# Optimization experiments

Measured on AMD Instinct MI355X. Metric: run time of the kernel, lower is better.

Reference implementation:

```python
import jax, jax.numpy as jnp
import numpy as np


def setup_inputs() -> dict:
    key = jax.random.key(0)
    ks = jax.random.split(key, 5)
    B, C_in, C_out, H, W, k = 16, 64, 64, 256, 256, 16
    scale = 1.0 / (C_in * C_out)
    return {
        "u": jax.random.normal(ks[0], (B, C_in, H, W), dtype=jnp.float32),
        "W_pos_re": scale * jax.random.normal(ks[1], (C_in, C_out, k, k), dtype=jnp.float32),
        "W_pos_im": scale * jax.random.normal(ks[2], (C_in, C_out, k, k), dtype=jnp.float32),
        "W_neg_re": scale * jax.random.normal(ks[3], (C_in, C_out, k, k), dtype=jnp.float32),
        "W_neg_im": scale * jax.random.normal(ks[4], (C_in, C_out, k, k), dtype=jnp.float32),
    }


def reference(u, W_pos_re, W_pos_im, W_neg_re, W_neg_im):
    B, C_in, H, W = u.shape
    C_out = W_pos_re.shape[1]
    k = W_pos_re.shape[2]
    W_half = W // 2 + 1
    k_h = min(k, H // 2)
    k_w = min(k, W_half)

    R_pos = (W_pos_re + 1j * W_pos_im)[:, :, :k_h, :k_w]  # (C_in, C_out, k_h, k_w)
    R_neg = (W_neg_re + 1j * W_neg_im)[:, :, :k_h, :k_w]

    u_hat = jnp.fft.rfft2(u, norm="ortho")  # (B, C_in, H, W_half) complex

    # spectral multiply on retained modes only
    top = jnp.einsum("bchw,cohw->bohw", u_hat[:, :, :k_h, :k_w], R_pos)
    bot = jnp.einsum("bchw,cohw->bohw", u_hat[:, :, H - k_h:, :k_w], R_neg)

    v_hat = jnp.zeros((B, C_out, H, W_half), dtype=u_hat.dtype)
    v_hat = v_hat.at[:, :, :k_h, :k_w].set(top)
    v_hat = v_hat.at[:, :, H - k_h:, :k_w].set(bot)

    return jnp.fft.irfft2(v_hat, s=(H, W), norm="ortho")  # (B, C_out, H, W) real
```

## Files before the change

kernel.cpp:

```cpp
#include <hip/hip_runtime.h>


#define OFF_CT 0
#define OFF_ST 256
#define OFF_RP 512
#define RP_SZ  (512*4096*2)
#define OFF_U  (OFF_RP + RP_SZ)
#define U_SZ   (1024*512*2)
#define OFF_V  (OFF_U + U_SZ)

#define UTP   260
#define TWOPI_256 0.024543692606170259f

typedef const __attribute__((address_space(1))) void g_void;
typedef __attribute__((address_space(3))) void l_void;

__device__ __forceinline__ void load_lds16(const float* g, float* l) {
    __builtin_amdgcn_global_load_lds((g_void*)g, (l_void*)l, 16, 0, 0);
}

template<int CTRL>
__device__ __forceinline__ float dppf(float x) {
    return __int_as_float(__builtin_amdgcn_update_dpp(
        0, __float_as_int(x), CTRL, 0xF, 0xF, true));
}

__global__ __launch_bounds__(256) void k_fwd1(const float* __restrict__ u,
                                              const float* __restrict__ wpr,
                                              const float* __restrict__ wpi,
                                              const float* __restrict__ wnr,
                                              const float* __restrict__ wni,
                                              float* __restrict__ ws,
                                              float* __restrict__ P) {
    __shared__ __align__(16) float ut[32][UTP];
    int t = threadIdx.x;

    if (blockIdx.x >= 8192) {
        int mw = blockIdx.x - 8192;
        int m = mw >> 4, wmc = mw & 15;
        const float* wr; const float* wi; int i;
        if (m < 16) { wr = wpr; wi = wpi; i = m; }
        else        { wr = wnr; wi = wni; i = m - 16; }
        if (mw == 0) {
            double a = 2.0 * 3.14159265358979323846 * (double)t / 256.0;
            ws[OFF_CT + t] = (float)cos(a);
            ws[OFF_ST + t] = (float)sin(a);
        }
        float norm = (wmc == 0 ? 1.f : 2.f) * (1.f / 65536.f);
        int off = i * 16 + wmc;
        float2* rp = (float2*)(ws + OFF_RP) + (size_t)mw * 4096;
        #pragma unroll
        for (int k = 0; k < 16; ++k) {
            int co = t + 256 * k;
            rp[co] = make_float2(wr[(size_t)co * 256 + off] * norm,
                                 wi[(size_t)co * 256 + off] * norm);
        }
        return;
    }

    int bc = blockIdx.x >> 3, ch = blockIdx.x & 7;
    const float* ub = u + (size_t)bc * 65536 + ch * 8192;
    int lane = t & 63, w = t >> 6;
    #pragma unroll
    for (int k = 0; k < 8; ++k)
        load_lds16(ub + (w * 8 + k) * 256 + lane * 4, &ut[w * 8 + k][0]);

    int s = lane & 3, h = (lane >> 2) & 1, r8 = lane >> 3;
    int rowc = w * 8 + r8;

    float sv, cv;
    __sincosf(TWOPI_256 * 1.f, &sv, &cv);
    float rb1r = cv, rb1i = -sv;
    __sincosf(TWOPI_256 * (float)(8 * h), &sv, &cv);
    float r8hr = cv, r8hi = -sv;
    int j0 = 16 * s;
    __sincosf(TWOPI_256 * (float)((8 * h * j0) & 255), &sv, &cv);
    float tw0r = cv, tw0i = -sv;
    __sincosf(TWOPI_256 * (float)j0, &sv, &cv);
    float bjr = cv, bji = -sv;

    float a0r=0,a0i=0,a1r=0,a1i=0,a2r=0,a2i=0,a3r=0,a3i=0;
    float a4r=0,a4i=0,a5r=0,a5i=0,a6r=0,a6i=0,a7r=0,a7i=0;

    asm volatile("s_waitcnt vmcnt(0)" ::: "memory");

    const float* q0p = &ut[rowc][j0];
    #define CMUL_(tr_, ti_) { float nr_ = tr_*bjr - ti_*bji,                \
          ni_ = tr_*bji + ti_*bjr; tr_ = nr_; ti_ = ni_; }
    #define STEP_(u0,u1,u2,u3) {                                            \
        float Av_=(u0)+(u2), Bv_=(u1)+(u3), Cv_=(u0)-(u2), Dv_=(u1)-(u3);   \
        float gp_ = Av_ + Bv_, gm_ = Av_ - Bv_;                             \
        float twr = tw0r, twi = tw0i;                                       \
        a0r = fmaf(gp_, twr, a0r); a0i = fmaf(gp_, twi, a0i);               \
        CMUL_(twr, twi)                                                     \
        a1r = fmaf(Cv_, twr, fmaf( Dv_, twi, a1r));                         \
        a1i = fmaf(Cv_, twi, fmaf(-Dv_, twr, a1i));                         \
        CMUL_(twr, twi)                                                     \
        a2r = fmaf(gm_, twr, a2r); a2i = fmaf(gm_, twi, a2i);               \
        CMUL_(twr, twi)                                                     \
        a3r = fmaf(Cv_, twr, fmaf(-Dv_, twi, a3r));                         \
        a3i = fmaf(Cv_, twi, fmaf( Dv_, twr, a3i));                         \
        CMUL_(twr, twi)                                                     \
        a4r = fmaf(gp_, twr, a4r); a4i = fmaf(gp_, twi, a4i);               \
        CMUL_(twr, twi)                                                     \
        a5r = fmaf(Cv_, twr, fmaf( Dv_, twi, a5r));                         \
        a5i = fmaf(Cv_, twi, fmaf(-Dv_, twr, a5i));                         \
        CMUL_(twr, twi)                                                     \
        a6r = fmaf(gm_, twr, a6r); a6i = fmaf(gm_, twi, a6i);               \
        CMUL_(twr, twi)                                                     \
        a7r = fmaf(Cv_, twr, fmaf(-Dv_, twi, a7r));                         \
        a7i = fmaf(Cv_, twi, fmaf( Dv_, twr, a7i));                         \
        { float nr = tw0r*r8hr - tw0i*r8hi, ni = tw0r*r8hi + tw0i*r8hr;     \
          tw0r = nr; tw0i = ni; }                                           \
        { float nr = bjr*rb1r - bji*rb1i, ni = bjr*rb1i + bji*rb1r;         \
          bjr = nr; bji = ni; } }

    #pragma unroll
    for (int g = 0; g < 4; ++g) {
        float4 x0 = *(const float4*)(q0p + 4 * g);
        float4 x1 = *(const float4*)(q0p + 64  + 4 * g);
        float4 x2 = *(const float4*)(q0p + 128 + 4 * g);
        float4 x3 = *(const float4*)(q0p + 192 + 4 * g);
        STEP_(x0.x, x1.x, x2.x, x3.x)
        STEP_(x0.y, x1.y, x2.y, x3.y)
        STEP_(x0.z, x1.z, x2.z, x3.z)
        STEP_(x0.w, x1.w, x2.w, x3.w)
    }
    #undef STEP_
    #undef CMUL_

    #define RED_(v) { v += dppf<0xB1>(v); v += dppf<0x4E>(v); }
    RED_(a0r) RED_(a0i) RED_(a1r) RED_(a1i)
    RED_(a2r) RED_(a2i) RED_(a3r) RED_(a3i)
    RED_(a4r) RED_(a4i) RED_(a5r) RED_(a5i)
    RED_(a6r) RED_(a6i) RED_(a7r) RED_(a7i)
    #undef RED_

    if ((lane & 3) == 0) {
        int y = ch * 32 + rowc;
        float4* Pp = (float4*)P + (((size_t)bc * 256 + y) * 8 + 4 * h);
        Pp[0] = make_float4(a0r, a0i, a1r, a1i);
        Pp[1] = make_float4(a2r, a2i, a3r, a3i);
        Pp[2] = make_float4(a4r, a4i, a5r, a5i);
        Pp[3] = make_float4(a6r, a6i, a7r, a7i);
    }
}

__global__ __launch_bounds__(256) void k_fwd2(const float* __restrict__ P,
                                              float* __restrict__ ws) {
    __shared__ float Pl[256][36];
    int t = threadIdx.x, bc = blockIdx.x;
    const float4* Pg = (const float4*)(P + (size_t)bc * 8192);
    #pragma unroll
    for (int k = 0; k < 8; ++k) {
        int f4 = t + 256 * k;
        int y = f4 >> 3, q = f4 & 7;
        *(float4*)&Pl[y][q * 4] = Pg[f4];
    }
    __syncthreads();

    int wm = t & 15;
    int v  = t >> 4;
    int m1 = ((v & 3) << 2) | (v >> 2);
    float sv, cv;
    __sincosf(TWOPI_256 * (float)m1, &sv, &cv);
    float r1r = cv, r1i = -sv;
    __sincosf(TWOPI_256 * (float)(m1 - 16), &sv, &cv);
    float r2r = cv, r2i = -sv;
    float t1r = 1.f, t1i = 0.f, t2r = 1.f, t2i = 0.f;
    float U1r = 0.f, U1i = 0.f, U2r = 0.f, U2i = 0.f;
    int md = m1 & 3;
    #pragma unroll 4
    for (int yy = 0; yy < 64; ++yy) {
        float2 P0 = *(float2*)&Pl[yy][2 * wm];
        float2 P1 = *(float2*)&Pl[yy + 64][2 * wm];
        float2 P2 = *(float2*)&Pl[yy + 128][2 * wm];
        float2 P3 = *(float2*)&Pl[yy + 192][2 * wm];
        float ar = P0.x + P2.x, ai = P0.y + P2.y;
        float br = P1.x + P3.x, bi = P1.y + P3.y;
        float cr = P0.x - P2.x, ci = P0.y - P2.y;
        float dr = P1.x - P3.x, di = P1.y - P3.y;
        float gr, gi;
        if (md == 0)      { gr = ar + br; gi = ai + bi; }
        else if (md == 1) { gr = cr + di; gi = ci - dr; }
        else if (md == 2) { gr = ar - br; gi = ai - bi; }
        else              { gr = cr - di; gi = ci + dr; }
        U1r = fmaf(gr, t1r, fmaf(-gi, t1i, U1r));
        U1i = fmaf(gr, t1i, fmaf( gi, t1r, U1i));
        U2r = fmaf(gr, t2r, fmaf(-gi, t2i, U2r));
        U2i = fmaf(gr, t2i, fmaf( gi, t2r, U2i));
        float n1r = t1r * r1r - t1i * r1i, n1i = t1r * r1i + t1i * r1r;
        float n2r = t2r * r2r - t2i * r2i, n2i = t2r * r2i + t2i * r2r;
        t1r = n1r; t1i = n1i; t2r = n2r; t2i = n2i;
    }
    float2* U = (float2*)(ws + OFF_U) + (size_t)bc * 512;
    U[m1 * 16 + wm]          = make_float2(U1r, U1i);
    U[(m1 + 16) * 16 + wm]   = make_float2(U2r, U2i);
}

__global__ __launch_bounds__(256) void k_cgemm(float* __restrict__ ws) {
    __shared__ float2 Ul[1024];
    int mw = blockIdx.x, t = threadIdx.x;
    const float2* Ug = (const float2*)(ws + OFF_U);
    #pragma unroll
    for (int k = 0; k < 4; ++k) {
        int bcv = t + 256 * k;
        Ul[bcv] = Ug[(size_t)bcv * 512 + mw];
    }
    __syncthreads();
    int o = t & 63, bq = t >> 6;
    const float2* rp = (const float2*)(ws + OFF_RP) + (size_t)mw * 4096;
    float ar[4] = {0.f, 0.f, 0.f, 0.f}, ai[4] = {0.f, 0.f, 0.f, 0.f};
    #pragma unroll 4
    for (int c = 0; c < 64; ++c) {
        float2 R = rp[c * 64 + o];
        #pragma unroll
        for (int j = 0; j < 4; ++j) {
            float2 Uv = Ul[(bq * 4 + j) * 64 + c];
            ar[j] = fmaf(Uv.x, R.x, fmaf(-Uv.y, R.y, ar[j]));
            ai[j] = fmaf(Uv.x, R.y, fmaf( Uv.y, R.x, ai[j]));
        }
    }
    float2* Vg = (float2*)(ws + OFF_V) + (size_t)mw * 1024;
    #pragma unroll
    for (int j = 0; j < 4; ++j)
        Vg[(bq * 4 + j) * 64 + o] = make_float2(ar[j], ai[j]);
}

__global__ __launch_bounds__(256) void k_inv(const float* __restrict__ ws,
                                             float* __restrict__ out) {
    __shared__ float Vl[16][68];
    __shared__ float Tl[4][16][36];
    __shared__ float ct[256], st[256];
    int t = threadIdx.x;
    int bo = blockIdx.x >> 2, q = blockIdx.x & 3;
    ct[t] = ws[OFF_CT + t];
    st[t] = ws[OFF_ST + t];
    {
        const float2* Vg = (const float2*)(ws + OFF_V);
        float2 v0 = Vg[(size_t)t * 1024 + bo];
        float2 v1 = Vg[(size_t)(t + 256) * 1024 + bo];
        int m = t >> 4, wmv = t & 15;
        Vl[wmv][2 * m]        = v0.x;  Vl[wmv][2 * m + 1]        = v0.y;
        Vl[wmv][2 * (m + 16)] = v1.x;  Vl[wmv][2 * (m + 16) + 1] = v1.y;
    }
    __syncthreads();

    int wm4 = t & 15, yb = t >> 4;
    int y0 = q * 16 + yb;
    float vr[32], vi[32];
    #pragma unroll
    for (int m = 0; m < 32; ++m) { vr[m] = Vl[wm4][2 * m]; vi[m] = Vl[wm4][2 * m + 1]; }
    float cy = ct[y0], sy = st[y0];
    float T0r=0,T0i=0,T1r=0,T1i=0,T2r=0,T2i=0,T3r=0,T3i=0;
    float tr = 1.f, ti = 0.f;
    #pragma unroll
    for (int m = 0; m < 32; ++m) {
        if (m == 16) {
            int i16 = (4096 - 16 * y0) & 255;
            tr = ct[i16]; ti = st[i16];
        }
        float hr = vr[m] * tr - vi[m] * ti;
        float hi = vr[m] * ti + vi[m] * tr;
        const int md = m & 3;
        T0r += hr; T0i += hi;
        if (md == 0)      { T1r += hr; T1i += hi; T2r += hr; T2i += hi; T3r += hr; T3i += hi; }
        else if (md == 1) { T1r -= hi; T1i += hr; T2r -= hr; T2i -= hi; T3r += hi; T3i -= hr; }
        else if (md == 2) { T1r -= hr; T1i -= hi; T2r += hr; T2i += hi; T3r -= hr; T3i -= hi; }
        else              { T1r += hi; T1i -= hr; T2r -= hr; T2i -= hi; T3r -= hi; T3i += hr; }
        float nr = tr * cy - ti * sy, ni = tr * sy + ti * cy;
        tr = nr; ti = ni;
    }
    Tl[0][yb][wm4] = T0r; Tl[0][yb][16 + wm4] = T0i;
    Tl[1][yb][wm4] = T1r; Tl[1][yb][16 + wm4] = T1i;
    Tl[2][yb][wm4] = T2r; Tl[2][yb][16 + wm4] = T2i;
    Tl[3][yb][wm4] = T3r; Tl[3][yb][16 + wm4] = T3i;
    __syncthreads();

    int l = t & 63, wv = t >> 6;
    float c0[16], s0[16];
    #pragma unroll
    for (int wm = 0; wm < 16; ++wm) {
        int idx = (wm * l) & 255;
        c0[wm] = ct[idx]; s0[wm] = st[idx];
    }
    float* ob = out + (size_t)bo * 65536;
    for (int yi = 0; yi < 16; ++yi) {
        int y = wv * 64 + q * 16 + yi;
        float TR[16], TI[16];
        const float4* rowv = (const float4*)&Tl[wv][yi][0];
        #pragma unroll
        for (int qq = 0; qq < 4; ++qq) {
            float4 a = rowv[qq];
            TR[4*qq]=a.x; TR[4*qq+1]=a.y; TR[4*qq+2]=a.z; TR[4*qq+3]=a.w;
            float4 b = rowv[qq + 4];
            TI[4*qq]=b.x; TI[4*qq+1]=b.y; TI[4*qq+2]=b.z; TI[4*qq+3]=b.w;
        }
        float Pv = 0.f, Qv = 0.f, Rv = 0.f, Sv = 0.f;
        #pragma unroll
        for (int wm = 0; wm < 16; wm += 2) {
            Pv = fmaf(TR[wm],     c0[wm],     Pv);
            Rv = fmaf(TI[wm],     s0[wm],     Rv);
            Qv = fmaf(TR[wm + 1], c0[wm + 1], Qv);
            Sv = fmaf(TI[wm + 1], s0[wm + 1], Sv);
        }
        float Ac = Pv + Qv, Bs = Rv + Sv;
        float Dc = Pv - Qv, Es = Rv - Sv;
        float* row = ob + (size_t)y * 256;
        row[l]               = Ac - Bs;
        row[(256 - l) & 255] = Ac + Bs;
        row[128 + l]         = Dc - Es;
        row[128 - l]         = Dc + Es;
        float E0 = TR[0] + TR[4] + TR[8]  + TR[12];
        float E2 = TR[2] + TR[6] + TR[10] + TR[14];
        float O1 = TI[1] + TI[5] + TI[9]  + TI[13];
        float O3 = TI[3] + TI[7] + TI[11] + TI[15];
        float EC = E0 - E2, OC = O1 - O3;
        if (l == 0) {
            row[64]  = EC - OC;
            row[192] = EC + OC;
        }
    }
}

extern "C" void kernel_launch(void* const* d_in, const int* in_sizes, int n_in,
                              void* d_out, int out_size, void* d_ws, size_t ws_size,
                              hipStream_t stream) {
    const float* u   = (const float*)d_in[0];
    const float* wpr = (const float*)d_in[1];
    const float* wpi = (const float*)d_in[2];
    const float* wnr = (const float*)d_in[3];
    const float* wni = (const float*)d_in[4];
    float* out = (float*)d_out;
    float* ws  = (float*)d_ws;
    float* P   = (float*)d_out;

    hipLaunchKernelGGL(k_fwd1,  dim3(8704), dim3(256), 0, stream, u, wpr, wpi, wnr, wni, ws, P);
    hipLaunchKernelGGL(k_fwd2,  dim3(1024), dim3(256), 0, stream, P, ws);
    hipLaunchKernelGGL(k_cgemm, dim3(512),  dim3(256), 0, stream, ws);
    hipLaunchKernelGGL(k_inv,   dim3(4096), dim3(256), 0, stream, ws, out);
}
```

Before: 204.7 us.

## Fuse column DFT stage into forward row-DFT kernel with partial sums

Removes the separate k_fwd2 kernel. Each k_fwd1 block now does its 32-row slice of the column DFT directly from shared memory and writes per-chunk partial spectra. k_cgemm sums the 8 partial chunks while loading. This drops one kernel launch and the round trip of the full row-DFT intermediate through global memory. In exchange, the partial-sum buffer is 8x the size of the retained spectrum, cgemm does extra strided loads, and the fwd1 blocks get extra shared memory and a sync.

```diff
diff --git a/kernel.cpp b/kernel.cpp
--- a/kernel.cpp
+++ b/kernel.cpp
@@ -5,9 +5,7 @@
 #define OFF_ST 256
 #define OFF_RP 512
 #define RP_SZ  (512*4096*2)
-#define OFF_U  (OFF_RP + RP_SZ)
-#define U_SZ   (1024*512*2)
-#define OFF_V  (OFF_U + U_SZ)
+#define OFF_V  (OFF_RP + RP_SZ)
 
 #define UTP   260
 #define TWOPI_256 0.024543692606170259f
@@ -31,8 +29,9 @@
                                               const float* __restrict__ wnr,
                                               const float* __restrict__ wni,
                                               float* __restrict__ ws,
-                                              float* __restrict__ P) {
+                                              float* __restrict__ Upart) {
     __shared__ __align__(16) float ut[32][UTP];
+    __shared__ __align__(16) float Pl[32][36];
     int t = threadIdx.x;
 
     if (blockIdx.x >= 8192) {
@@ -82,6 +81,15 @@
     float a0r=0,a0i=0,a1r=0,a1i=0,a2r=0,a2i=0,a3r=0,a3i=0;
     float a4r=0,a4i=0,a5r=0,a5i=0,a6r=0,a6i=0,a7r=0,a7i=0;
 
+    int wm2 = t & 15, m1 = t >> 4;
+    __sincosf(TWOPI_256 * (float)m1, &sv, &cv);
+    float q1r = cv, q1i = -sv;
+    __sincosf(TWOPI_256 * (float)(m1 - 16), &sv, &cv);
+    float q2r = cv, q2i = -sv;
+    __sincosf(TWOPI_256 * (float)((m1 * 32 * ch) & 255), &sv, &cv);
+    float w1r = cv, w1i = -sv;
+    float w2r = w1r, w2i = w1i;
+
     asm volatile("s_waitcnt vmcnt(0)" ::: "memory");
 
     const float* q0p = &ut[rowc][j0];
@@ -137,75 +145,46 @@
     #undef RED_
 
     if ((lane & 3) == 0) {
-        int y = ch * 32 + rowc;
-        float4* Pp = (float4*)P + (((size_t)bc * 256 + y) * 8 + 4 * h);
+        float4* Pp = (float4*)&Pl[rowc][16 * h];
         Pp[0] = make_float4(a0r, a0i, a1r, a1i);
         Pp[1] = make_float4(a2r, a2i, a3r, a3i);
         Pp[2] = make_float4(a4r, a4i, a5r, a5i);
         Pp[3] = make_float4(a6r, a6i, a7r, a7i);
     }
-}
-
-__global__ __launch_bounds__(256) void k_fwd2(const float* __restrict__ P,
-                                              float* __restrict__ ws) {
-    __shared__ float Pl[256][36];
-    int t = threadIdx.x, bc = blockIdx.x;
-    const float4* Pg = (const float4*)(P + (size_t)bc * 8192);
-    #pragma unroll
-    for (int k = 0; k < 8; ++k) {
-        int f4 = t + 256 * k;
-        int y = f4 >> 3, q = f4 & 7;
-        *(float4*)&Pl[y][q * 4] = Pg[f4];
-    }
     __syncthreads();
 
-    int wm = t & 15;
-    int v  = t >> 4;
-    int m1 = ((v & 3) << 2) | (v >> 2);
-    float sv, cv;
-    __sincosf(TWOPI_256 * (float)m1, &sv, &cv);
-    float r1r = cv, r1i = -sv;
-    __sincosf(TWOPI_256 * (float)(m1 - 16), &sv, &cv);
-    float r2r = cv, r2i = -sv;
-    float t1r = 1.f, t1i = 0.f, t2r = 1.f, t2i = 0.f;
     float U1r = 0.f, U1i = 0.f, U2r = 0.f, U2i = 0.f;
-    int md = m1 & 3;
     #pragma unroll 4
-    for (int yy = 0; yy < 64; ++yy) {
-        float2 P0 = *(float2*)&Pl[yy][2 * wm];
-        float2 P1 = *(float2*)&Pl[yy + 64][2 * wm];
-        float2 P2 = *(float2*)&Pl[yy + 128][2 * wm];
-        float2 P3 = *(float2*)&Pl[yy + 192][2 * wm];
-        float ar = P0.x + P2.x, ai = P0.y + P2.y;
-        float br = P1.x + P3.x, bi = P1.y + P3.y;
-        float cr = P0.x - P2.x, ci = P0.y - P2.y;
-        float dr = P1.x - P3.x, di = P1.y - P3.y;
-        float gr, gi;
-        if (md == 0)      { gr = ar + br; gi = ai + bi; }
-        else if (md == 1) { gr = cr + di; gi = ci - dr; }
-        else if (md == 2) { gr = ar - br; gi = ai - bi; }
-        else              { gr = cr - di; gi = ci + dr; }
-        U1r = fmaf(gr, t1r, fmaf(-gi, t1i, U1r));
-        U1i = fmaf(gr, t1i, fmaf( gi, t1r, U1i));
-        U2r = fmaf(gr, t2r, fmaf(-gi, t2i, U2r));
-        U2i = fmaf(gr, t2i, fmaf( gi, t2r, U2i));
-        float n1r = t1r * r1r - t1i * r1i, n1i = t1r * r1i + t1i * r1r;
-        float n2r = t2r * r2r - t2i * r2i, n2i = t2r * r2i + t2i * r2r;
-        t1r = n1r; t1i = n1i; t2r = n2r; t2i = n2i;
-    }
-    float2* U = (float2*)(ws + OFF_U) + (size_t)bc * 512;
-    U[m1 * 16 + wm]          = make_float2(U1r, U1i);
-    U[(m1 + 16) * 16 + wm]   = make_float2(U2r, U2i);
-}
-
-__global__ __launch_bounds__(256) void k_cgemm(float* __restrict__ ws) {
+    for (int yy = 0; yy < 32; ++yy) {
+        float2 g = *(float2*)&Pl[yy][2 * wm2];
+        U1r = fmaf(g.x, w1r, fmaf(-g.y, w1i, U1r));
+        U1i = fmaf(g.x, w1i, fmaf( g.y, w1r, U1i));
+        U2r = fmaf(g.x, w2r, fmaf(-g.y, w2i, U2r));
+        U2i = fmaf(g.x, w2i, fmaf( g.y, w2r, U2i));
+        float n1r = w1r * q1r - w1i * q1i, n1i = w1r * q1i + w1i * q1r;
+        float n2r = w2r * q2r - w2i * q2i, n2i = w2r * q2i + w2i * q2r;
+        w1r = n1r; w1i = n1i; w2r = n2r; w2i = n2i;
+    }
+    float2* Ug = (float2*)Upart + ((size_t)(ch * 1024 + bc)) * 512;
+    Ug[t]       = make_float2(U1r, U1i);
+    Ug[t + 256] = make_float2(U2r, U2i);
+}
+
+__global__ __launch_bounds__(256) void k_cgemm(const float* __restrict__ Upart,
+                                               float* __restrict__ ws) {
     __shared__ float2 Ul[1024];
     int mw = blockIdx.x, t = threadIdx.x;
-    const float2* Ug = (const float2*)(ws + OFF_U);
+    const float2* Ug = (const float2*)Upart;
     #pragma unroll
     for (int k = 0; k < 4; ++k) {
         int bcv = t + 256 * k;
-        Ul[bcv] = Ug[(size_t)bcv * 512 + mw];
+        float sr = 0.f, si = 0.f;
+        #pragma unroll
+        for (int ch = 0; ch < 8; ++ch) {
+            float2 v = Ug[((size_t)(ch * 1024 + bcv)) * 512 + mw];
+            sr += v.x; si += v.y;
+        }
+        Ul[bcv] = make_float2(sr, si);
     }
     __syncthreads();
     int o = t & 63, bq = t >> 6;
@@ -333,10 +312,9 @@
     const float* wni = (const float*)d_in[4];
     float* out = (float*)d_out;
     float* ws  = (float*)d_ws;
-    float* P   = (float*)d_out;
-
-    hipLaunchKernelGGL(k_fwd1,  dim3(8704), dim3(256), 0, stream, u, wpr, wpi, wnr, wni, ws, P);
-    hipLaunchKernelGGL(k_fwd2,  dim3(1024), dim3(256), 0, stream, P, ws);
-    hipLaunchKernelGGL(k_cgemm, dim3(512),  dim3(256), 0, stream, ws);
+    float* Upart = (float*)d_out;
+
+    hipLaunchKernelGGL(k_fwd1,  dim3(8704), dim3(256), 0, stream, u, wpr, wpi, wnr, wni, ws, Upart);
+    hipLaunchKernelGGL(k_cgemm, dim3(512),  dim3(256), 0, stream, Upart, ws);
     hipLaunchKernelGGL(k_inv,   dim3(4096), dim3(256), 0, stream, ws, out);
 }
```

Result: slower. 250.3 us (+22.3%).
